# Kernel tuning notes

Hardware: AMD Instinct MI355X
Metric: run time of the kernel (lower is better)

## Reference

```python
import jax, jax.numpy as jnp
import numpy as np
import math

B, T, H, NH, BLOCK = 2, 2048, 1024, 16, 2048
HS = H // NH  # 64, even as required by RoPE


def make_rope_cache(hs, block):
    # positions t = 1..block (note: source starts at 1, not 0)
    t = np.arange(1, block + 1, dtype=np.float32)[:, None]          # (block, 1)
    i = np.arange(1, hs // 2 + 1, dtype=np.float32)[None, :]        # (1, hs/2)
    theta = (1.0 / 10000.0) ** (2.0 * (i - 1.0) / hs)               # (1, hs/2)
    ang = t * theta                                                  # (block, hs/2)
    return jnp.asarray(np.stack([np.cos(ang), np.sin(ang)], axis=-1))  # (block, hs/2, 2)


def setup_inputs() -> dict:
    key = jax.random.key(0)
    ks = jax.random.split(key, 10)
    s = 0.02
    x = jax.random.normal(ks[0], (B, T, H), jnp.float32)
    masks = jax.random.randint(ks[1], (B, T), 0, 2, jnp.int32)  # 1 = padding token
    Wq = jax.random.normal(ks[2], (H, H), jnp.float32) * s
    bq = jnp.zeros((H,), jnp.float32)
    Wk = jax.random.normal(ks[3], (H, H), jnp.float32) * s
    bk = jnp.zeros((H,), jnp.float32)
    Wv = jax.random.normal(ks[4], (H, H), jnp.float32) * s
    bv = jnp.zeros((H,), jnp.float32)
    Wo = jax.random.normal(ks[5], (H, H), jnp.float32) * s  # final_proj, no bias
    rope = make_rope_cache(HS, BLOCK)
    return {"x": x, "masks": masks, "Wq": Wq, "bq": bq, "Wk": Wk, "bk": bk,
            "Wv": Wv, "bv": bv, "Wo": Wo, "rope": rope}


def _apply_rope(x, cos, sin):
    # x: (B, nh, T, hs); cos/sin: (T, hs/2) broadcast over (B, nh)
    xe, xo = x[..., ::2], x[..., 1::2]
    real = cos * xe - sin * xo
    imag = sin * xe + cos * xo
    return jnp.stack([real, imag], axis=-1).reshape(x.shape)


def reference(x, masks, Wq, bq, Wk, bk, Wv, bv, Wo, rope):
    Bn, Tn, Hn = x.shape
    nh, hs = NH, Hn // NH

    def proj(W, b):
        # torch Linear: x @ W.T + b -> (B, nh, T, hs)
        return (x @ W.T + b).reshape(Bn, Tn, nh, hs).transpose(0, 2, 1, 3)

    Q, K, V = proj(Wq, bq), proj(Wk, bk), proj(Wv, bv)
    cos, sin = rope[:Tn, :, 0], rope[:Tn, :, 1]
    Q = _apply_rope(Q, cos, sin)
    K = _apply_rope(K, cos, sin)

    att = jnp.einsum('bhqd,bhkd->bhqk', Q, K) * (1.0 / math.sqrt(hs))
    causal = jnp.tril(jnp.ones((Tn, Tn), bool))
    att = jnp.where(causal[None, None, :, :], att, -1e10)          # causal mask
    att = jnp.where((masks == 1)[:, None, None, :], -1e10, att)   # padding mask on keys
    att = jax.nn.softmax(att, axis=-1)

    y = jnp.einsum('bhqk,bhkd->bhqd', att, V)
    y = y.transpose(0, 2, 1, 3).reshape(Bn, Tn, Hn)
    return y @ Wo.T  # final_proj has no bias
```

## Files before the change

kernel.cpp:

```cpp
#include <hip/hip_runtime.h>

typedef short short8 __attribute__((ext_vector_type(8)));
typedef float floatx4 __attribute__((ext_vector_type(4)));
typedef unsigned short u16;
typedef unsigned long long u64;

#define Tn 2048
#define Kdim 1024
#define QSCALE 0.18033688011112042f
#define FIXEDMAX 20.0f

__device__ inline u16 f2bf(float x) {
    union { float f; unsigned u; } c; c.f = x;
    unsigned u = c.u;
    u += 0x7fffu + ((u >> 16) & 1u);
    return (u16)(u >> 16);
}
__device__ inline float bf2f(u16 h) {
    union { unsigned u; float f; } c; c.u = ((unsigned)h) << 16;
    return c.f;
}
__device__ inline floatx4 mfma16(short8 a, short8 b, floatx4 c) {
    return __builtin_amdgcn_mfma_f32_16x16x32_bf16(a, b, c, 0, 0, 0);
}
__device__ inline void async16(const void* g, void* l) {
    __builtin_amdgcn_global_load_lds((const __attribute__((address_space(1))) void*)g,
                                     (__attribute__((address_space(3))) void*)l, 16, 0, 0);
}

__global__ __launch_bounds__(256) void cvt_all_k(
    const float* __restrict__ x, const float* __restrict__ wq, const float* __restrict__ wk,
    const float* __restrict__ wv, const float* __restrict__ wo, u16* __restrict__ dst)
{
    int i = blockIdx.x * 256 + threadIdx.x;
    const float* s; int off;
    if (i < 1048576) { s = x; off = i; }
    else {
        int j = i - 1048576; int seg = j >> 18; off = j & 262143;
        s = (seg == 0) ? wq : (seg == 1) ? wk : (seg == 2) ? wv : wo;
    }
    float4 v = ((const float4*)s)[off];
    u64 pk = (u64)f2bf(v.x) | ((u64)f2bf(v.y) << 16) | ((u64)f2bf(v.z) << 32) | ((u64)f2bf(v.w) << 48);
    ((u64*)dst)[i] = pk;
}

__global__ __launch_bounds__(256, 5) void gemm_qkv_k(
    const u16* __restrict__ A,
    const u16* __restrict__ W0, const u16* __restrict__ W1, const u16* __restrict__ W2,
    const float* __restrict__ b0, const float* __restrict__ b1, const float* __restrict__ b2,
    u16* o0, u16* o1, u16* o2,
    const float2* __restrict__ rope)
{
    int z = blockIdx.z;
    const u16* W = (z == 0) ? W0 : (z == 1 ? W1 : W2);
    const float* bias = (z == 0) ? b0 : (z == 1 ? b1 : b2);
    u16* outp = (z == 0) ? o0 : (z == 1 ? o1 : o2);

    __shared__ __align__(16) char lds[24576];
    int tid = threadIdx.x;
    int w = tid >> 6, lane = tid & 63, quad = lane >> 4, l15 = lane & 15;
    int m0 = blockIdx.y * 128, n0 = blockIdx.x * 64;
    int wm = w * 32;

    floatx4 acc[2][4];
    floatx4 vzero = {0.f, 0.f, 0.f, 0.f};
#pragma unroll
    for (int i = 0; i < 2; ++i)
#pragma unroll
        for (int j = 0; j < 4; ++j) acc[i][j] = vzero;

    for (int k0 = 0; k0 < Kdim; k0 += 64) {
#pragma unroll
        for (int j = 0; j < 4; ++j) {
            int f = j * 256 + tid, r = f >> 3, c = (f & 7) ^ (r & 7);
            async16(A + (size_t)(m0 + r) * Kdim + k0 + c * 8, lds + j * 4096 + w * 1024);
        }
#pragma unroll
        for (int j = 0; j < 2; ++j) {
            int f = j * 256 + tid, r = f >> 3, c = (f & 7) ^ (r & 7);
            async16(W + (size_t)(n0 + r) * Kdim + k0 + c * 8, lds + 16384 + j * 4096 + w * 1024);
        }
        __syncthreads();
        short8 af[2][2];
#pragma unroll
        for (int mt = 0; mt < 2; ++mt) {
            int ra = wm + mt * 16 + l15;
            const char* pa = lds + ra * 128;
#pragma unroll
            for (int ks = 0; ks < 2; ++ks)
                af[mt][ks] = *(const short8*)(pa + (((ks * 4 + quad) ^ (ra & 7)) << 4));
        }
#pragma unroll
        for (int ks = 0; ks < 2; ++ks)
#pragma unroll
            for (int nt = 0; nt < 4; ++nt) {
                int rb = nt * 16 + l15;
                short8 bf = *(const short8*)(lds + 16384 + rb * 128 + (((ks * 4 + quad) ^ (rb & 7)) << 4));
                acc[0][nt] = mfma16(af[0][ks], bf, acc[0][nt]);
                acc[1][nt] = mfma16(af[1][ks], bf, acc[1][nt]);
            }
        __syncthreads();
    }

    int mbase = m0 + wm;
    if (z <= 1) {
        float osc = (z == 0) ? QSCALE : 1.0f;
#pragma unroll
        for (int nt = 0; nt < 4; ++nt) {
            int col = n0 + nt * 16 + l15;
            float bv = bias[col];
            int p = (col & 63) >> 1;
#pragma unroll
            for (int mt = 0; mt < 2; ++mt) {
                floatx4 a = acc[mt][nt];
#pragma unroll
                for (int r = 0; r < 4; ++r) {
                    int row = mbase + mt * 16 + quad * 4 + r;
                    float v = a[r] + bv;
                    float ov = __shfl_xor(v, 1, 64);
                    float2 cs = rope[(row & (Tn - 1)) * 32 + p];
                    float res = (cs.x * v + ((lane & 1) ? cs.y * ov : -cs.y * ov)) * osc;
                    float pres = __shfl_xor(res, 1, 64);
                    if (!(lane & 1)) {
                        unsigned pk = (unsigned)f2bf(res) | ((unsigned)f2bf(pres) << 16);
                        *(unsigned*)(outp + (size_t)row * 1024 + col) = pk;
                    }
                }
            }
        }
    } else {
#pragma unroll
        for (int nt = 0; nt < 4; ++nt) {
            int col = n0 + nt * 16 + l15;
            float bv = bias[col];
#pragma unroll
            for (int mt = 0; mt < 2; ++mt) {
                floatx4 a = acc[mt][nt];
                int row0 = mbase + mt * 16 + quad * 4;
                int bb = row0 >> 11, t0 = row0 & (Tn - 1);
                u64 pk = (u64)f2bf(a[0] + bv) | ((u64)f2bf(a[1] + bv) << 16)
                       | ((u64)f2bf(a[2] + bv) << 32) | ((u64)f2bf(a[3] + bv) << 48);
                *(u64*)(outp + (size_t)(bb * 1024 + col) * Tn + t0) = pk;
            }
        }
    }
}

__global__ __launch_bounds__(256, 4) void gemm_o_k(
    const u16* __restrict__ A, const u16* __restrict__ W, float* __restrict__ out)
{
    __shared__ __align__(16) char lds[16384];
    int tid = threadIdx.x;
    int w = tid >> 6, lane = tid & 63, quad = lane >> 4, l15 = lane & 15;
    int m0 = blockIdx.y * 64, n0 = blockIdx.x * 64;
    int wm = (w >> 1) * 32, wn = (w & 1) * 32;

    floatx4 acc[2][2];
    floatx4 vzero = {0.f, 0.f, 0.f, 0.f};
#pragma unroll
    for (int i = 0; i < 2; ++i)
#pragma unroll
        for (int j = 0; j < 2; ++j) acc[i][j] = vzero;

    for (int k0 = 0; k0 < Kdim; k0 += 64) {
#pragma unroll
        for (int j = 0; j < 2; ++j) {
            int f = j * 256 + tid, r = f >> 3, c = (f & 7) ^ (r & 7);
            async16(A + (size_t)(m0 + r) * Kdim + k0 + c * 8, lds + j * 4096 + w * 1024);
            async16(W + (size_t)(n0 + r) * Kdim + k0 + c * 8, lds + 8192 + j * 4096 + w * 1024);
        }
        __syncthreads();
        short8 af[2][2];
#pragma unroll
        for (int mt = 0; mt < 2; ++mt) {
            int ra = wm + mt * 16 + l15;
            const char* pa = lds + ra * 128;
#pragma unroll
            for (int ks = 0; ks < 2; ++ks)
                af[mt][ks] = *(const short8*)(pa + (((ks * 4 + quad) ^ (ra & 7)) << 4));
        }
#pragma unroll
        for (int ks = 0; ks < 2; ++ks)
#pragma unroll
            for (int nt = 0; nt < 2; ++nt) {
                int rb = wn + nt * 16 + l15;
                short8 bf = *(const short8*)(lds + 8192 + rb * 128 + (((ks * 4 + quad) ^ (rb & 7)) << 4));
                acc[0][nt] = mfma16(af[0][ks], bf, acc[0][nt]);
                acc[1][nt] = mfma16(af[1][ks], bf, acc[1][nt]);
            }
        __syncthreads();
    }

#pragma unroll
    for (int nt = 0; nt < 2; ++nt) {
        int col = n0 + wn + nt * 16 + l15;
#pragma unroll
        for (int mt = 0; mt < 2; ++mt) {
            floatx4 a = acc[mt][nt];
#pragma unroll
            for (int r = 0; r < 4; ++r) {
                int row = m0 + wm + mt * 16 + quad * 4 + r;
                out[(size_t)row * 1024 + col] = a[r];
            }
        }
    }
}

__global__ __launch_bounds__(64) void vmean_k(const u16* __restrict__ Vt, float* __restrict__ vmean) {
    int row = blockIdx.x;
    int lane = threadIdx.x;
    const u16* p = Vt + (size_t)row * Tn;
    float s = 0.f;
    for (int i = lane * 8; i < Tn; i += 512) {
        short8 v = *(const short8*)(p + i);
#pragma unroll
        for (int j = 0; j < 8; ++j) s += bf2f((u16)v[j]);
    }
#pragma unroll
    for (int off = 1; off < 64; off <<= 1) s += __shfl_xor(s, off, 64);
    if (lane == 0) vmean[row] = s * (1.f / 2048.f);
}

__global__ __launch_bounds__(256) void flash_k(
    const u16* __restrict__ Qb, const u16* __restrict__ Kb, const u16* __restrict__ Vt,
    const int* __restrict__ masks, const float* __restrict__ vmean, u16* __restrict__ Yb)
{
    int bid = blockIdx.x;
    int bh = (bid & 7) * 4 + ((bid >> 3) & 3);
    int qt = 31 - (bid >> 5);
    int b = bh >> 4, h = bh & 15;
    int tid = threadIdx.x, w = tid >> 6, lane = tid & 63, quad = lane >> 4, l15 = lane & 15;
    int sc = (lane & 7) ^ (lane >> 3);

    __shared__ __align__(16) u16 ldsK[2][64 * 64];
    __shared__ __align__(16) u16 ldsV[2][64 * 64];
    __shared__ __align__(16) u16 ldsP[4][16 * 64];

    int ktiles = qt + 1;
    unsigned blo = 0, bhi = 0;
    for (int j = 0; j < ktiles; ++j) {
        u64 mk = __ballot(masks[b * Tn + j * 64 + lane] != 0);
        if (lane == j) { blo = (unsigned)mk; bhi = (unsigned)(mk >> 32); }
    }

    auto stage = [&](int bb, int k0) {
#pragma unroll
        for (int j = 0; j < 2; ++j) {
            int row = j * 32 + w * 8 + (lane >> 3);
            const u16* gk = Kb + (size_t)(b * Tn + k0 + row) * 1024 + h * 64 + sc * 8;
            async16(gk, (char*)&ldsK[bb][0] + (j * 32 + w * 8) * 128);
            const u16* gv = Vt + (size_t)(b * 1024 + h * 64 + row) * Tn + k0 + sc * 8;
            async16(gv, (char*)&ldsV[bb][0] + (j * 32 + w * 8) * 128);
        }
    };
    floatx4 vzero = {0.f, 0.f, 0.f, 0.f};

    int q0 = qt * 64 + w * 16;
    short8 qf[2];
    {
        const u16* qp = Qb + (size_t)(b * Tn + q0 + l15) * 1024 + h * 64 + quad * 8;
        qf[0] = *(const short8*)qp;
        qf[1] = *(const short8*)(qp + 32);
    }
    floatx4 o[4];
    float lsum[4] = {0.f, 0.f, 0.f, 0.f};
#pragma unroll
    for (int i = 0; i < 4; ++i) o[i] = vzero;

    stage(0, 0);
    for (int kt = 0; kt < ktiles; ++kt) {
        int k0 = kt * 64;
        int bb = kt & 1;
        __syncthreads();

        short8 kf[4][2], vf[4][2];
#pragma unroll
        for (int f = 0; f < 4; ++f) {
            int key = f * 16 + l15;
            const char* kbase = (const char*)&ldsK[bb][0] + key * 128;
            const char* vbase = (const char*)&ldsV[bb][0] + key * 128;
#pragma unroll
            for (int ks = 0; ks < 2; ++ks) {
                int slot = ((quad + ks * 4) ^ (key & 7)) << 4;
                kf[f][ks] = *(const short8*)(kbase + slot);
                vf[f][ks] = *(const short8*)(vbase + slot);
            }
        }
        if (kt + 1 < ktiles) stage(bb ^ 1, k0 + 64);

        floatx4 s[4];
#pragma unroll
        for (int f = 0; f < 4; ++f) {
            s[f] = mfma16(qf[0], kf[f][0], vzero);
            s[f] = mfma16(qf[1], kf[f][1], s[f]);
        }

        unsigned mlo = __shfl(blo, kt, 64), mhi = __shfl(bhi, kt, 64);
        int mb[4];
        mb[0] = (mlo >> l15) & 1; mb[1] = (mlo >> (l15 + 16)) & 1;
        mb[2] = (mhi >> l15) & 1; mb[3] = (mhi >> (l15 + 16)) & 1;

        if (k0 + 63 <= q0) {
#pragma unroll
            for (int r = 0; r < 4; ++r) {
                float psum = 0.f;
#pragma unroll
                for (int f = 0; f < 4; ++f) {
                    float v = mb[f] ? -1e10f : s[f][r];
                    float p = __builtin_amdgcn_exp2f(v - FIXEDMAX);
                    psum += p;
                    unsigned u = __float_as_uint(p) + 0x8000u;
                    int row = quad * 4 + r, key = f * 16 + l15;
                    ldsP[w][0] = ldsP[w][0];
                    *((u16*)((char*)&ldsP[w][0] + row * 128 +
                             ((((key >> 3) ^ (row & 7))) << 4) + (key & 7) * 2)) = (u16)(u >> 16);
                }
                lsum[r] += psum;
            }
        } else {
#pragma unroll
            for (int r = 0; r < 4; ++r) {
                int lim = q0 + quad * 4 + r - k0;
                float psum = 0.f;
#pragma unroll
                for (int f = 0; f < 4; ++f) {
                    float v = (16 * f + l15 > lim || mb[f]) ? -1e10f : s[f][r];
                    float p = __builtin_amdgcn_exp2f(v - FIXEDMAX);
                    psum += p;
                    unsigned u = __float_as_uint(p) + 0x8000u;
                    int row = quad * 4 + r, key = f * 16 + l15;
                    *((u16*)((char*)&ldsP[w][0] + row * 128 +
                             ((((key >> 3) ^ (row & 7))) << 4) + (key & 7) * 2)) = (u16)(u >> 16);
                }
                lsum[r] += psum;
            }
        }
        __asm__ volatile("s_waitcnt lgkmcnt(0)" ::: "memory");
        short8 pf0 = *(const short8*)((const char*)&ldsP[w][0] + l15 * 128 + ((quad ^ (l15 & 7)) << 4));
        short8 pf1 = *(const short8*)((const char*)&ldsP[w][0] + l15 * 128 + (((quad + 4) ^ (l15 & 7)) << 4));
#pragma unroll
        for (int nb = 0; nb < 4; ++nb) {
            o[nb] = mfma16(pf0, vf[nb][0], o[nb]);
            o[nb] = mfma16(pf1, vf[nb][1], o[nb]);
        }
    }

#pragma unroll
    for (int r = 0; r < 4; ++r) {
        int qq = q0 + quad * 4 + r;
        float l = lsum[r];
#pragma unroll
        for (int off = 1; off < 16; off <<= 1) l += __shfl_xor(l, off, 64);
        bool degen = (l == 0.f);
        float linv = 1.0f / l;
#pragma unroll
        for (int nb = 0; nb < 4; ++nb) {
            int d = nb * 16 + l15;
            float val = degen ? vmean[b * 1024 + h * 64 + d] : o[nb][r] * linv;
            float pv = __shfl_xor(val, 1, 64);
            if (!(lane & 1)) {
                unsigned pk = (unsigned)f2bf(val) | ((unsigned)f2bf(pv) << 16);
                *(unsigned*)(Yb + (size_t)(b * Tn + qq) * 1024 + h * 64 + d) = pk;
            }
        }
    }
}

extern "C" void kernel_launch(void* const* d_in, const int* in_sizes, int n_in,
                              void* d_out, int out_size, void* d_ws, size_t ws_size,
                              hipStream_t stream) {
    const float* x  = (const float*)d_in[0];
    const int* masks = (const int*)d_in[1];
    const float* Wq = (const float*)d_in[2];
    const float* bq = (const float*)d_in[3];
    const float* Wk = (const float*)d_in[4];
    const float* bk = (const float*)d_in[5];
    const float* Wv = (const float*)d_in[6];
    const float* bv = (const float*)d_in[7];
    const float* Wo = (const float*)d_in[8];
    const float2* rope = (const float2*)d_in[9];
    float* out = (float*)d_out;

    char* ws = (char*)d_ws;
    u16* xb   = (u16*)(ws);
    u16* Wqb  = (u16*)(ws + (8  << 20));
    u16* Wkb  = (u16*)(ws + (10 << 20));
    u16* Wvb  = (u16*)(ws + (12 << 20));
    u16* Wob  = (u16*)(ws + (14 << 20));
    u16* Qb   = (u16*)(ws + (16 << 20));
    u16* Kb2  = (u16*)(ws + (24 << 20));
    u16* Vt   = (u16*)(ws + (32 << 20));
    u16* Yb   = (u16*)(ws + (40 << 20));
    float* vm = (float*)(ws + (48 << 20));

    cvt_all_k<<<8192, 256, 0, stream>>>(x, Wq, Wk, Wv, Wo, xb);

    gemm_qkv_k<<<dim3(16, 32, 3), 256, 0, stream>>>(xb, Wqb, Wkb, Wvb, bq, bk, bv,
                                                    Qb, Kb2, Vt, rope);
    vmean_k<<<2048, 64, 0, stream>>>(Vt, vm);
    flash_k<<<1024, 256, 0, stream>>>(Qb, Kb2, Vt, masks, vm, Yb);
    gemm_o_k<<<dim3(16, 64), 256, 0, stream>>>(Yb, Wob, out);
}
```

Measured before the change: 193.6 us.

## Split long causal query tiles across two blocks and merge partials in finisher

Query tiles 16-31 have their key range split in half across two blocks, which write bf16 partial outputs and row sums to scratch. A new fin_k kernel combines the halves, normalizes them, and falls back to vmean for rows whose keys are all masked. The padding mask and fixed-max offset are now loaded into the MFMA accumulator init, which removes per-element selects on tiles that are not on the diagonal. The aim is to balance causal work across more blocks, at the cost of an extra launch, scratch traffic and bf16 rounding of the partials. gemm_o_k's occupancy hint is also raised.

```diff
diff --git a/kernel.cpp b/kernel.cpp
--- a/kernel.cpp
+++ b/kernel.cpp
@@ -146,7 +146,7 @@
     }
 }
 
-__global__ __launch_bounds__(256, 4) void gemm_o_k(
+__global__ __launch_bounds__(256, 6) void gemm_o_k(
     const u16* __restrict__ A, const u16* __restrict__ W, float* __restrict__ out)
 {
     __shared__ __align__(16) char lds[16384];
@@ -223,11 +223,25 @@
 
 __global__ __launch_bounds__(256) void flash_k(
     const u16* __restrict__ Qb, const u16* __restrict__ Kb, const u16* __restrict__ Vt,
-    const int* __restrict__ masks, const float* __restrict__ vmean, u16* __restrict__ Yb)
+    const int* __restrict__ masks, const float* __restrict__ vmean, u16* __restrict__ Yb,
+    u16* __restrict__ oP, float* __restrict__ lS)
 {
     int bid = blockIdx.x;
-    int bh = (bid & 7) * 4 + ((bid >> 3) & 3);
-    int qt = 31 - (bid >> 5);
+    int qt, bh, half, kt0, kt1, split;
+    if (bid < 1024) {
+        qt = 31 - (bid >> 6);
+        bh = (bid & 7) * 4 + ((bid >> 3) & 3);
+        half = (bid >> 5) & 1;
+        int h0 = (qt + 1) >> 1;
+        kt0 = half ? h0 : 0;
+        kt1 = half ? (qt + 1) : h0;
+        split = 1;
+    } else {
+        int j = bid - 1024;
+        qt = 15 - (j >> 5);
+        bh = (j & 7) * 4 + ((j >> 3) & 3);
+        half = 0; kt0 = 0; kt1 = qt + 1; split = 0;
+    }
     int b = bh >> 4, h = bh & 15;
     int tid = threadIdx.x, w = tid >> 6, lane = tid & 63, quad = lane >> 4, l15 = lane & 15;
     int sc = (lane & 7) ^ (lane >> 3);
@@ -236,9 +250,8 @@
     __shared__ __align__(16) u16 ldsV[2][64 * 64];
     __shared__ __align__(16) u16 ldsP[4][16 * 64];
 
-    int ktiles = qt + 1;
     unsigned blo = 0, bhi = 0;
-    for (int j = 0; j < ktiles; ++j) {
+    for (int j = kt0; j < kt1; ++j) {
         u64 mk = __ballot(masks[b * Tn + j * 64 + lane] != 0);
         if (lane == j) { blo = (unsigned)mk; bhi = (unsigned)(mk >> 32); }
     }
@@ -267,10 +280,10 @@
 #pragma unroll
     for (int i = 0; i < 4; ++i) o[i] = vzero;
 
-    stage(0, 0);
-    for (int kt = 0; kt < ktiles; ++kt) {
+    stage(0, kt0 * 64);
+    for (int kt = kt0; kt < kt1; ++kt) {
         int k0 = kt * 64;
-        int bb = kt & 1;
+        int bb = (kt - kt0) & 1;
         __syncthreads();
 
         short8 kf[4][2], vf[4][2];
@@ -286,46 +299,35 @@
                 vf[f][ks] = *(const short8*)(vbase + slot);
             }
         }
-        if (kt + 1 < ktiles) stage(bb ^ 1, k0 + 64);
-
+        if (kt + 1 < kt1) stage(bb ^ 1, k0 + 64);
+
+        unsigned mlo = __shfl(blo, kt, 64), mhi = __shfl(bhi, kt, 64);
         floatx4 s[4];
+        {
+            float m0i = ((mlo >> l15) & 1) ? -1.0e10f : -FIXEDMAX;
+            float m1i = ((mlo >> (l15 + 16)) & 1) ? -1.0e10f : -FIXEDMAX;
+            float m2i = ((mhi >> l15) & 1) ? -1.0e10f : -FIXEDMAX;
+            float m3i = ((mhi >> (l15 + 16)) & 1) ? -1.0e10f : -FIXEDMAX;
+            s[0] = (floatx4){m0i, m0i, m0i, m0i};
+            s[1] = (floatx4){m1i, m1i, m1i, m1i};
+            s[2] = (floatx4){m2i, m2i, m2i, m2i};
+            s[3] = (floatx4){m3i, m3i, m3i, m3i};
+        }
 #pragma unroll
         for (int f = 0; f < 4; ++f) {
-            s[f] = mfma16(qf[0], kf[f][0], vzero);
+            s[f] = mfma16(qf[0], kf[f][0], s[f]);
             s[f] = mfma16(qf[1], kf[f][1], s[f]);
         }
 
-        unsigned mlo = __shfl(blo, kt, 64), mhi = __shfl(bhi, kt, 64);
-        int mb[4];
-        mb[0] = (mlo >> l15) & 1; mb[1] = (mlo >> (l15 + 16)) & 1;
-        mb[2] = (mhi >> l15) & 1; mb[3] = (mhi >> (l15 + 16)) & 1;
-
-        if (k0 + 63 <= q0) {
-#pragma unroll
-            for (int r = 0; r < 4; ++r) {
-                float psum = 0.f;
-#pragma unroll
-                for (int f = 0; f < 4; ++f) {
-                    float v = mb[f] ? -1e10f : s[f][r];
-                    float p = __builtin_amdgcn_exp2f(v - FIXEDMAX);
-                    psum += p;
-                    unsigned u = __float_as_uint(p) + 0x8000u;
-                    int row = quad * 4 + r, key = f * 16 + l15;
-                    ldsP[w][0] = ldsP[w][0];
-                    *((u16*)((char*)&ldsP[w][0] + row * 128 +
-                             ((((key >> 3) ^ (row & 7))) << 4) + (key & 7) * 2)) = (u16)(u >> 16);
-                }
-                lsum[r] += psum;
-            }
-        } else {
+        if (kt == qt) {
 #pragma unroll
             for (int r = 0; r < 4; ++r) {
                 int lim = q0 + quad * 4 + r - k0;
                 float psum = 0.f;
 #pragma unroll
                 for (int f = 0; f < 4; ++f) {
-                    float v = (16 * f + l15 > lim || mb[f]) ? -1e10f : s[f][r];
-                    float p = __builtin_amdgcn_exp2f(v - FIXEDMAX);
+                    float v = (16 * f + l15 > lim) ? -1.0e10f : s[f][r];
+                    float p = __builtin_amdgcn_exp2f(v);
                     psum += p;
                     unsigned u = __float_as_uint(p) + 0x8000u;
                     int row = quad * 4 + r, key = f * 16 + l15;
@@ -334,6 +336,21 @@
                 }
                 lsum[r] += psum;
             }
+        } else {
+#pragma unroll
+            for (int r = 0; r < 4; ++r) {
+                float psum = 0.f;
+#pragma unroll
+                for (int f = 0; f < 4; ++f) {
+                    float p = __builtin_amdgcn_exp2f(s[f][r]);
+                    psum += p;
+                    unsigned u = __float_as_uint(p) + 0x8000u;
+                    int row = quad * 4 + r, key = f * 16 + l15;
+                    *((u16*)((char*)&ldsP[w][0] + row * 128 +
+                             ((((key >> 3) ^ (row & 7))) << 4) + (key & 7) * 2)) = (u16)(u >> 16);
+                }
+                lsum[r] += psum;
+            }
         }
         __asm__ volatile("s_waitcnt lgkmcnt(0)" ::: "memory");
         short8 pf0 = *(const short8*)((const char*)&ldsP[w][0] + l15 * 128 + ((quad ^ (l15 & 7)) << 4));
@@ -345,25 +362,75 @@
         }
     }
 
-#pragma unroll
-    for (int r = 0; r < 4; ++r) {
-        int qq = q0 + quad * 4 + r;
-        float l = lsum[r];
-#pragma unroll
-        for (int off = 1; off < 16; off <<= 1) l += __shfl_xor(l, off, 64);
-        bool degen = (l == 0.f);
-        float linv = 1.0f / l;
-#pragma unroll
-        for (int nb = 0; nb < 4; ++nb) {
-            int d = nb * 16 + l15;
-            float val = degen ? vmean[b * 1024 + h * 64 + d] : o[nb][r] * linv;
-            float pv = __shfl_xor(val, 1, 64);
-            if (!(lane & 1)) {
-                unsigned pk = (unsigned)f2bf(val) | ((unsigned)f2bf(pv) << 16);
-                *(unsigned*)(Yb + (size_t)(b * Tn + qq) * 1024 + h * 64 + d) = pk;
-            }
-        }
-    }
+    if (!split) {
+#pragma unroll
+        for (int r = 0; r < 4; ++r) {
+            int qq = q0 + quad * 4 + r;
+            float l = lsum[r];
+#pragma unroll
+            for (int off = 1; off < 16; off <<= 1) l += __shfl_xor(l, off, 64);
+            bool degen = (l == 0.f);
+            float linv = 1.0f / l;
+#pragma unroll
+            for (int nb = 0; nb < 4; ++nb) {
+                int d = nb * 16 + l15;
+                float val = degen ? vmean[b * 1024 + h * 64 + d] : o[nb][r] * linv;
+                float pv = __shfl_xor(val, 1, 64);
+                if (!(lane & 1)) {
+                    unsigned pk = (unsigned)f2bf(val) | ((unsigned)f2bf(pv) << 16);
+                    *(unsigned*)(Yb + (size_t)(b * Tn + qq) * 1024 + h * 64 + d) = pk;
+                }
+            }
+        }
+    } else {
+        int sq = (qt - 16) * 32 + bh;
+        u16* ob = oP + (size_t)(half * 512 + sq) * 4096;
+        float* lb = lS + (size_t)(half * 512 + sq) * 64;
+#pragma unroll
+        for (int r = 0; r < 4; ++r) {
+            int q = w * 16 + quad * 4 + r;
+            float l = lsum[r];
+#pragma unroll
+            for (int off = 1; off < 16; off <<= 1) l += __shfl_xor(l, off, 64);
+            if (l15 == 0) lb[q] = l;
+#pragma unroll
+            for (int nb = 0; nb < 4; ++nb) {
+                int d = nb * 16 + l15;
+                float val = o[nb][r];
+                float pv = __shfl_xor(val, 1, 64);
+                if (!(lane & 1)) {
+                    unsigned pk = (unsigned)f2bf(val) | ((unsigned)f2bf(pv) << 16);
+                    *(unsigned*)(ob + q * 64 + d) = pk;
+                }
+            }
+        }
+    }
+}
+
+__global__ __launch_bounds__(256) void fin_k(
+    const u16* __restrict__ oP, const float* __restrict__ lS,
+    const float* __restrict__ vmean, u16* __restrict__ Yb)
+{
+    int blk = blockIdx.x;
+    int sq = blk >> 2, qg = blk & 3;
+    int qt = 16 + (sq >> 5), bh = sq & 31, b = bh >> 4, h = bh & 15;
+    int tid = threadIdx.x;
+    int q = qg * 16 + (tid >> 4);
+    int d0 = (tid & 15) * 4;
+    u64 ua = *(const u64*)(oP + (size_t)sq * 4096 + q * 64 + d0);
+    u64 ub = *(const u64*)(oP + (size_t)(512 + sq) * 4096 + q * 64 + d0);
+    float l = lS[sq * 64 + q] + lS[(512 + sq) * 64 + q];
+    bool degen = (l == 0.f);
+    float linv = 1.0f / l;
+    u64 outp = 0;
+#pragma unroll
+    for (int i = 0; i < 4; ++i) {
+        float va = bf2f((u16)(ua >> (16 * i))), vb = bf2f((u16)(ub >> (16 * i)));
+        float val = degen ? vmean[b * 1024 + h * 64 + d0 + i] : (va + vb) * linv;
+        outp |= (u64)f2bf(val) << (16 * i);
+    }
+    int qrow = qt * 64 + q;
+    *(u64*)(Yb + (size_t)(b * Tn + qrow) * 1024 + h * 64 + d0) = outp;
 }
 
 extern "C" void kernel_launch(void* const* d_in, const int* in_sizes, int n_in,
@@ -392,12 +459,15 @@
     u16* Vt   = (u16*)(ws + (32 << 20));
     u16* Yb   = (u16*)(ws + (40 << 20));
     float* vm = (float*)(ws + (48 << 20));
+    u16* oP   = (u16*)(ws);
+    float* lS = (float*)(ws + (8 << 20));
 
     cvt_all_k<<<8192, 256, 0, stream>>>(x, Wq, Wk, Wv, Wo, xb);
 
     gemm_qkv_k<<<dim3(16, 32, 3), 256, 0, stream>>>(xb, Wqb, Wkb, Wvb, bq, bk, bv,
                                                     Qb, Kb2, Vt, rope);
     vmean_k<<<2048, 64, 0, stream>>>(Vt, vm);
-    flash_k<<<1024, 256, 0, stream>>>(Qb, Kb2, Vt, masks, vm, Yb);
+    flash_k<<<1536, 256, 0, stream>>>(Qb, Kb2, Vt, masks, vm, Yb, oP, lS);
+    fin_k<<<2048, 256, 0, stream>>>(oP, lS, vm, Yb);
     gemm_o_k<<<dim3(16, 64), 256, 0, stream>>>(Yb, Wob, out);
 }
```

Result: slower. 209.0 us (+8.0%).

## Restructure flash attention to 2-wave blocks with direct global K/V loads

Applied to the files above, without the earlier changes.

Each flash attention block now runs 2 waves instead of 4, and each wave handles 32 query rows in two 16-row sub-tiles, so every K/V fragment it loads is used twice. K and V fragments are read straight from global memory into registers, replacing the LDS double-buffered async staging and its __syncthreads. The padding-mask offset and the fixed max are folded into the MFMA accumulator init, and the block-wide causal test is reduced to a diagonal-tile flag. The trade-off is heavier register pressure and no cross-wave sharing of K/V through LDS, so global and cache traffic rise. The output GEMM's launch-bounds occupancy hint is also raised.

```diff
diff --git a/kernel.cpp b/kernel.cpp
--- a/kernel.cpp
+++ b/kernel.cpp
@@ -146,7 +146,7 @@
     }
 }
 
-__global__ __launch_bounds__(256, 4) void gemm_o_k(
+__global__ __launch_bounds__(256, 6) void gemm_o_k(
     const u16* __restrict__ A, const u16* __restrict__ W, float* __restrict__ out)
 {
     __shared__ __align__(16) char lds[16384];
@@ -221,149 +221,149 @@
     if (lane == 0) vmean[row] = s * (1.f / 2048.f);
 }
 
-__global__ __launch_bounds__(256) void flash_k(
+__global__ __launch_bounds__(128) void flash_k(
     const u16* __restrict__ Qb, const u16* __restrict__ Kb, const u16* __restrict__ Vt,
     const int* __restrict__ masks, const float* __restrict__ vmean, u16* __restrict__ Yb)
 {
     int bid = blockIdx.x;
     int bh = (bid & 7) * 4 + ((bid >> 3) & 3);
-    int qt = 31 - (bid >> 5);
+    int blkq = 31 - (bid >> 5);
     int b = bh >> 4, h = bh & 15;
     int tid = threadIdx.x, w = tid >> 6, lane = tid & 63, quad = lane >> 4, l15 = lane & 15;
-    int sc = (lane & 7) ^ (lane >> 3);
-
-    __shared__ __align__(16) u16 ldsK[2][64 * 64];
-    __shared__ __align__(16) u16 ldsV[2][64 * 64];
-    __shared__ __align__(16) u16 ldsP[4][16 * 64];
-
-    int ktiles = qt + 1;
+
+    __shared__ __align__(16) u16 ldsP[2][16 * 64];
+
+    int qs = blkq * 64 + w * 32;
+    int ktiles = (qs >> 6) + 1;
+
+    int mv[32];
+#pragma unroll
+    for (int j = 0; j < 32; ++j) mv[j] = masks[b * Tn + j * 64 + lane];
     unsigned blo = 0, bhi = 0;
-    for (int j = 0; j < ktiles; ++j) {
-        u64 mk = __ballot(masks[b * Tn + j * 64 + lane] != 0);
+#pragma unroll
+    for (int j = 0; j < 32; ++j) {
+        u64 mk = __ballot(mv[j] != 0);
         if (lane == j) { blo = (unsigned)mk; bhi = (unsigned)(mk >> 32); }
     }
 
-    auto stage = [&](int bb, int k0) {
-#pragma unroll
-        for (int j = 0; j < 2; ++j) {
-            int row = j * 32 + w * 8 + (lane >> 3);
-            const u16* gk = Kb + (size_t)(b * Tn + k0 + row) * 1024 + h * 64 + sc * 8;
-            async16(gk, (char*)&ldsK[bb][0] + (j * 32 + w * 8) * 128);
-            const u16* gv = Vt + (size_t)(b * 1024 + h * 64 + row) * Tn + k0 + sc * 8;
-            async16(gv, (char*)&ldsV[bb][0] + (j * 32 + w * 8) * 128);
-        }
-    };
-    floatx4 vzero = {0.f, 0.f, 0.f, 0.f};
-
-    int q0 = qt * 64 + w * 16;
-    short8 qf[2];
-    {
-        const u16* qp = Qb + (size_t)(b * Tn + q0 + l15) * 1024 + h * 64 + quad * 8;
-        qf[0] = *(const short8*)qp;
-        qf[1] = *(const short8*)(qp + 32);
-    }
-    floatx4 o[4];
-    float lsum[4] = {0.f, 0.f, 0.f, 0.f};
-#pragma unroll
-    for (int i = 0; i < 4; ++i) o[i] = vzero;
-
-    stage(0, 0);
+    short8 qf[2][2];
+#pragma unroll
+    for (int s2 = 0; s2 < 2; ++s2) {
+        const u16* qp = Qb + (size_t)(b * Tn + qs + s2 * 16 + l15) * 1024 + h * 64 + quad * 8;
+        qf[s2][0] = *(const short8*)qp;
+        qf[s2][1] = *(const short8*)(qp + 32);
+    }
+
+    floatx4 o[2][4];
+    float lsum[2][4];
+#pragma unroll
+    for (int s2 = 0; s2 < 2; ++s2)
+#pragma unroll
+        for (int i = 0; i < 4; ++i) { o[s2][i] = (floatx4){0.f, 0.f, 0.f, 0.f}; lsum[s2][i] = 0.f; }
+
+    const u16* ku = Kb + (size_t)b * Tn * 1024 + h * 64;
+    const u16* vu = Vt + ((size_t)b * 1024 + h * 64) * Tn;
+    int klo = l15 * 1024 + quad * 8;
+    int vlo = l15 * Tn + quad * 8;
+    int pswz = l15 >> 3, pbyte = (l15 & 7) * 2;
+
     for (int kt = 0; kt < ktiles; ++kt) {
-        int k0 = kt * 64;
-        int bb = kt & 1;
-        __syncthreads();
-
         short8 kf[4][2], vf[4][2];
 #pragma unroll
         for (int f = 0; f < 4; ++f) {
-            int key = f * 16 + l15;
-            const char* kbase = (const char*)&ldsK[bb][0] + key * 128;
-            const char* vbase = (const char*)&ldsV[bb][0] + key * 128;
 #pragma unroll
             for (int ks = 0; ks < 2; ++ks) {
-                int slot = ((quad + ks * 4) ^ (key & 7)) << 4;
-                kf[f][ks] = *(const short8*)(kbase + slot);
-                vf[f][ks] = *(const short8*)(vbase + slot);
-            }
-        }
-        if (kt + 1 < ktiles) stage(bb ^ 1, k0 + 64);
-
-        floatx4 s[4];
-#pragma unroll
-        for (int f = 0; f < 4; ++f) {
-            s[f] = mfma16(qf[0], kf[f][0], vzero);
-            s[f] = mfma16(qf[1], kf[f][1], s[f]);
-        }
+                kf[f][ks] = *(const short8*)(ku + klo + f * 16 * 1024 + ks * 32);
+                vf[f][ks] = *(const short8*)(vu + vlo + f * 16 * Tn + ks * 32);
+            }
+        }
+        ku += 64 * 1024;
+        vu += 64;
 
         unsigned mlo = __shfl(blo, kt, 64), mhi = __shfl(bhi, kt, 64);
-        int mb[4];
-        mb[0] = (mlo >> l15) & 1; mb[1] = (mlo >> (l15 + 16)) & 1;
-        mb[2] = (mhi >> l15) & 1; mb[3] = (mhi >> (l15 + 16)) & 1;
-
-        if (k0 + 63 <= q0) {
-#pragma unroll
-            for (int r = 0; r < 4; ++r) {
-                float psum = 0.f;
-#pragma unroll
-                for (int f = 0; f < 4; ++f) {
-                    float v = mb[f] ? -1e10f : s[f][r];
-                    float p = __builtin_amdgcn_exp2f(v - FIXEDMAX);
-                    psum += p;
-                    unsigned u = __float_as_uint(p) + 0x8000u;
-                    int row = quad * 4 + r, key = f * 16 + l15;
-                    ldsP[w][0] = ldsP[w][0];
-                    *((u16*)((char*)&ldsP[w][0] + row * 128 +
-                             ((((key >> 3) ^ (row & 7))) << 4) + (key & 7) * 2)) = (u16)(u >> 16);
+        float mi[4];
+        mi[0] = ((mlo >> l15) & 1) ? -1.0e10f : -FIXEDMAX;
+        mi[1] = ((mlo >> (l15 + 16)) & 1) ? -1.0e10f : -FIXEDMAX;
+        mi[2] = ((mhi >> l15) & 1) ? -1.0e10f : -FIXEDMAX;
+        mi[3] = ((mhi >> (l15 + 16)) & 1) ? -1.0e10f : -FIXEDMAX;
+
+        floatx4 sA[2][4];
+#pragma unroll
+        for (int s2 = 0; s2 < 2; ++s2)
+#pragma unroll
+            for (int f = 0; f < 4; ++f) {
+                floatx4 c = (floatx4){mi[f], mi[f], mi[f], mi[f]};
+                c = mfma16(qf[s2][0], kf[f][0], c);
+                sA[s2][f] = mfma16(qf[s2][1], kf[f][1], c);
+            }
+
+        bool diag = (kt == ktiles - 1);
+#pragma unroll
+        for (int s2 = 0; s2 < 2; ++s2) {
+            char* pb = (char*)&ldsP[w][0];
+            if (diag) {
+#pragma unroll
+                for (int r = 0; r < 4; ++r) {
+                    int row = quad * 4 + r;
+                    int lim = qs + s2 * 16 + row - (kt << 6);
+                    float ps = 0.f;
+#pragma unroll
+                    for (int f = 0; f < 4; ++f) {
+                        float v = (f * 16 + l15 > lim) ? -1.0e10f : sA[s2][f][r];
+                        float p = __builtin_amdgcn_exp2f(v);
+                        ps += p;
+                        unsigned u = __float_as_uint(p) + 0x8000u;
+                        *(u16*)(pb + row * 128 + (((2 * f + pswz) ^ (row & 7)) << 4) + pbyte) = (u16)(u >> 16);
+                    }
+                    lsum[s2][r] += ps;
                 }
-                lsum[r] += psum;
-            }
-        } else {
-#pragma unroll
-            for (int r = 0; r < 4; ++r) {
-                int lim = q0 + quad * 4 + r - k0;
-                float psum = 0.f;
-#pragma unroll
-                for (int f = 0; f < 4; ++f) {
-                    float v = (16 * f + l15 > lim || mb[f]) ? -1e10f : s[f][r];
-                    float p = __builtin_amdgcn_exp2f(v - FIXEDMAX);
-                    psum += p;
-                    unsigned u = __float_as_uint(p) + 0x8000u;
-                    int row = quad * 4 + r, key = f * 16 + l15;
-                    *((u16*)((char*)&ldsP[w][0] + row * 128 +
-                             ((((key >> 3) ^ (row & 7))) << 4) + (key & 7) * 2)) = (u16)(u >> 16);
+            } else {
+#pragma unroll
+                for (int r = 0; r < 4; ++r) {
+                    int row = quad * 4 + r;
+                    float ps = 0.f;
+#pragma unroll
+                    for (int f = 0; f < 4; ++f) {
+                        float p = __builtin_amdgcn_exp2f(sA[s2][f][r]);
+                        ps += p;
+                        unsigned u = __float_as_uint(p) + 0x8000u;
+                        *(u16*)(pb + row * 128 + (((2 * f + pswz) ^ (row & 7)) << 4) + pbyte) = (u16)(u >> 16);
+                    }
+                    lsum[s2][r] += ps;
                 }
-                lsum[r] += psum;
-            }
-        }
-        __asm__ volatile("s_waitcnt lgkmcnt(0)" ::: "memory");
-        short8 pf0 = *(const short8*)((const char*)&ldsP[w][0] + l15 * 128 + ((quad ^ (l15 & 7)) << 4));
-        short8 pf1 = *(const short8*)((const char*)&ldsP[w][0] + l15 * 128 + (((quad + 4) ^ (l15 & 7)) << 4));
-#pragma unroll
-        for (int nb = 0; nb < 4; ++nb) {
-            o[nb] = mfma16(pf0, vf[nb][0], o[nb]);
-            o[nb] = mfma16(pf1, vf[nb][1], o[nb]);
-        }
-    }
-
-#pragma unroll
-    for (int r = 0; r < 4; ++r) {
-        int qq = q0 + quad * 4 + r;
-        float l = lsum[r];
-#pragma unroll
-        for (int off = 1; off < 16; off <<= 1) l += __shfl_xor(l, off, 64);
-        bool degen = (l == 0.f);
-        float linv = 1.0f / l;
-#pragma unroll
-        for (int nb = 0; nb < 4; ++nb) {
-            int d = nb * 16 + l15;
-            float val = degen ? vmean[b * 1024 + h * 64 + d] : o[nb][r] * linv;
-            float pv = __shfl_xor(val, 1, 64);
-            if (!(lane & 1)) {
-                unsigned pk = (unsigned)f2bf(val) | ((unsigned)f2bf(pv) << 16);
-                *(unsigned*)(Yb + (size_t)(b * Tn + qq) * 1024 + h * 64 + d) = pk;
-            }
-        }
-    }
+            }
+            __asm__ volatile("s_waitcnt lgkmcnt(0)" ::: "memory");
+            short8 pf0 = *(const short8*)(pb + l15 * 128 + ((quad ^ (l15 & 7)) << 4));
+            short8 pf1 = *(const short8*)(pb + l15 * 128 + (((quad + 4) ^ (l15 & 7)) << 4));
+#pragma unroll
+            for (int nb = 0; nb < 4; ++nb) {
+                o[s2][nb] = mfma16(pf0, vf[nb][0], o[s2][nb]);
+                o[s2][nb] = mfma16(pf1, vf[nb][1], o[s2][nb]);
+            }
+        }
+    }
+
+#pragma unroll
+    for (int s2 = 0; s2 < 2; ++s2)
+#pragma unroll
+        for (int r = 0; r < 4; ++r) {
+            int qq = qs + s2 * 16 + quad * 4 + r;
+            float l = lsum[s2][r];
+#pragma unroll
+            for (int off = 1; off < 16; off <<= 1) l += __shfl_xor(l, off, 64);
+            bool degen = (l == 0.f);
+            float linv = 1.0f / l;
+#pragma unroll
+            for (int nb = 0; nb < 4; ++nb) {
+                int d = nb * 16 + l15;
+                float val = degen ? vmean[b * 1024 + h * 64 + d] : o[s2][nb][r] * linv;
+                float pv = __shfl_xor(val, 1, 64);
+                if (!(lane & 1)) {
+                    unsigned pk = (unsigned)f2bf(val) | ((unsigned)f2bf(pv) << 16);
+                    *(unsigned*)(Yb + (size_t)(b * Tn + qq) * 1024 + h * 64 + d) = pk;
+                }
+            }
+        }
 }
 
 extern "C" void kernel_launch(void* const* d_in, const int* in_sizes, int n_in,
@@ -398,6 +398,6 @@
     gemm_qkv_k<<<dim3(16, 32, 3), 256, 0, stream>>>(xb, Wqb, Wkb, Wvb, bq, bk, bv,
                                                     Qb, Kb2, Vt, rope);
     vmean_k<<<2048, 64, 0, stream>>>(Vt, vm);
-    flash_k<<<1024, 256, 0, stream>>>(Qb, Kb2, Vt, masks, vm, Yb);
+    flash_k<<<1024, 128, 0, stream>>>(Qb, Kb2, Vt, masks, vm, Yb);
     gemm_o_k<<<dim3(16, 64), 256, 0, stream>>>(Yb, Wob, out);
 }
```

Result: slower. 230.7 us (+19.2%).
